# Kernel tuning notes

Hardware: AMD Instinct MI355X
Metric: run time of the kernel (lower is better)

## Reference

```python
import jax, jax.numpy as jnp
import numpy as np

N_NODES = 100000
N_EDGES = 3200000
IN_DIM = 512
HEADS = 4
C1 = 8   # conv1 per-head channels
C2 = 4   # conv2 per-head channels
OUT_DIM = 10
N_GRAPHS = 64
NEG_SLOPE = 0.2


def _leaky_relu(x):
    return jnp.where(x >= 0, x, NEG_SLOPE * x)


def gat_conv(x, src, dst, W, a_src, a_dst, b):
    """PyG GATConv (concat=True). x:[N,F], src/dst:[E], W:[F,H*C], a_*:[H,C], b:[H*C]."""
    N = x.shape[0]
    H, C = a_src.shape
    h = (x @ W).reshape(N, H, C)                      # [N,H,C]
    e_src = jnp.einsum('nhc,hc->nh', h, a_src)        # [N,H]
    e_dst = jnp.einsum('nhc,hc->nh', h, a_dst)
    e = _leaky_relu(e_src[src] + e_dst[dst])          # [E,H]
    # segment softmax over edges grouped by destination node
    m = jax.ops.segment_max(e, dst, num_segments=N)   # [N,H]
    ex = jnp.exp(e - m[dst])
    denom = jax.ops.segment_sum(ex, dst, num_segments=N)
    alpha = ex / (denom[dst] + 1e-16)                 # [E,H]
    out = jax.ops.segment_sum(h[src] * alpha[:, :, None], dst, num_segments=N)
    return out.reshape(N, H * C) + b


def setup_inputs() -> dict:
    key = jax.random.key(0)
    ks = jax.random.split(key, 16)
    x = jax.random.normal(ks[0], (N_NODES, IN_DIM), dtype=jnp.float32)
    edge_index = jax.random.randint(ks[1], (2, N_EDGES), 0, N_NODES, dtype=jnp.int64)
    batch = jnp.sort(jax.random.randint(ks[2], (N_NODES,), 0, N_GRAPHS, dtype=jnp.int64))
    def glorot(k, shape):
        fan_in = shape[0] if len(shape) == 2 else shape[-1]
        return jax.random.normal(k, shape, dtype=jnp.float32) * (1.0 / np.sqrt(fan_in))
    return {
        'x': x, 'edge_index': edge_index, 'batch': batch,
        'W1': glorot(ks[3], (IN_DIM, HEADS * C1)),
        'att_src1': glorot(ks[4], (HEADS, C1)),
        'att_dst1': glorot(ks[5], (HEADS, C1)),
        'b1': jnp.zeros((HEADS * C1,), jnp.float32),
        'W2': glorot(ks[6], (HEADS * C1, HEADS * C2)),
        'att_src2': glorot(ks[7], (HEADS, C2)),
        'att_dst2': glorot(ks[8], (HEADS, C2)),
        'b2': jnp.zeros((HEADS * C2,), jnp.float32),
        'Wf': glorot(ks[9], (HEADS * C2, OUT_DIM)),
        'bf': jnp.zeros((OUT_DIM,), jnp.float32),
    }


def reference(x, edge_index, batch, W1, att_src1, att_dst1, b1,
              W2, att_src2, att_dst2, b2, Wf, bf):
    N = x.shape[0]
    loops = jnp.arange(N, dtype=edge_index.dtype)     # add_self_loops=True
    src = jnp.concatenate([edge_index[0], loops])
    dst = jnp.concatenate([edge_index[1], loops])
    h = jax.nn.relu(gat_conv(x, src, dst, W1, att_src1, att_dst1, b1))
    h = jax.nn.relu(gat_conv(h, src, dst, W2, att_src2, att_dst2, b2))
    # global_mean_pool over graphs
    sums = jax.ops.segment_sum(h, batch, num_segments=N_GRAPHS)
    cnt = jax.ops.segment_sum(jnp.ones((N,), h.dtype), batch, num_segments=N_GRAPHS)
    pooled = sums / jnp.maximum(cnt, 1.0)[:, None]    # [G, 16]
    return pooled @ Wf + bf
```

## Files before the change

### kernel.cpp

```cpp
#include <hip/hip_runtime.h>


#define LRELU(v) ((v) >= 0.f ? (v) : 0.2f * (v))

__global__ __launch_bounds__(256) void k_bin(const int* __restrict__ ei,
                                             int2* __restrict__ stg,
                                             int* __restrict__ rcnt,
                                             int E0, int Etot, int nr, int cap) {
    __shared__ int cnt[1024];
    __shared__ int base[1024];
    const int t = threadIdx.x;
    for (int i = t; i < nr; i += 256) cnt[i] = 0;
    __syncthreads();
    const int e0 = blockIdx.x * 8192;
#pragma unroll 4
    for (int k = 0; k < 32; k++) {
        int e = e0 + k * 256 + t;
        if (e < Etot) {
            int d = (e < E0) ? ei[E0 + e] : (e - E0);
            atomicAdd(&cnt[d >> 8], 1);
        }
    }
    __syncthreads();
    for (int i = t; i < nr; i += 256) {
        int c = cnt[i];
        base[i] = c ? atomicAdd(&rcnt[i], c) : 0;
        cnt[i] = 0;
    }
    __syncthreads();
#pragma unroll 4
    for (int k = 0; k < 32; k++) {
        int e = e0 + k * 256 + t;
        if (e < Etot) {
            int s, d;
            if (e < E0) {
                s = ei[e];
                d = ei[E0 + e];
            } else {
                s = d = e - E0;
            }
            int r = d >> 8;
            int slot = base[r] + atomicAdd(&cnt[r], 1);
            stg[(size_t)r * cap + slot] = make_int2(s, d);
        }
    }
}

__global__ __launch_bounds__(512) void k_sort(const int2* __restrict__ stg,
                                              const int* __restrict__ rcnt,
                                              int* __restrict__ row_ptr,
                                              int* __restrict__ ssrc,
                                              int N, int Etot, int nr, int cap) {
    __shared__ int hist[256];
    __shared__ int hs[256];
    __shared__ int red[512];
    const int r = blockIdx.x;
    const int t = threadIdx.x;
    int part = 0;
    for (int i = t; i < r; i += 512) part += rcnt[i];
    red[t] = part;
    if (t < 256) hist[t] = 0;
    __syncthreads();
    for (int off = 256; off > 0; off >>= 1) {
        if (t < off) red[t] += red[t + off];
        __syncthreads();
    }
    const int rb = red[0];
    const int n0 = r << 8;
    const int cnt = rcnt[r];
    const int2* seg = stg + (size_t)r * cap;
    for (int i = t; i < cnt; i += 512) {
        int d = seg[i].y;
        atomicAdd(&hist[d - n0], 1);
    }
    __syncthreads();
    if (t < 256) hs[t] = hist[t];
    __syncthreads();
    for (int off = 1; off < 256; off <<= 1) {
        int o = (t < 256 && t >= off) ? hs[t - off] : 0;
        __syncthreads();
        if (t < 256) hs[t] += o;
        __syncthreads();
    }
    if (t < 256) {
        int excl = hs[t] - hist[t];
        int node = n0 + t;
        if (node < N) row_ptr[node] = rb + excl;
        hist[t] = excl;
    }
    if (r == nr - 1 && t == 0) row_ptr[N] = Etot;
    __syncthreads();
    for (int i = t; i < cnt; i += 512) {
        int2 sd2 = seg[i];
        int off = atomicAdd(&hist[sd2.y - n0], 1);
        ssrc[rb + off] = sd2.x;
    }
}

__global__ __launch_bounds__(256) void k_gemm1(const float* __restrict__ x,
                                               const float* __restrict__ W,
                                               const float* __restrict__ a_src,
                                               const float* __restrict__ a_dst,
                                               float* __restrict__ h,
                                               float* __restrict__ es,
                                               float* __restrict__ ed, int N) {
    __shared__ float xs[32 * 132];
    __shared__ float ws[32 * 36];
    const int t = threadIdx.x;
    const int r0 = (t >> 2) * 2;
    const int cg = t & 3;
    const int row0 = blockIdx.x * 128;

    float acc[2][8];
#pragma unroll
    for (int i = 0; i < 2; i++)
#pragma unroll
        for (int j = 0; j < 8; j++) acc[i][j] = 0.f;

    float4 xr[4];
    float4 wr;
    const int xrow = t >> 3, xc4 = t & 7;
    const int wk = t >> 3, wc4 = t & 7;

    auto load_chunk = [&](int kc) {
#pragma unroll
        for (int ii = 0; ii < 4; ii++) {
            int row = xrow + ii * 32;
            int rr = row0 + row;
            if (rr >= N) rr = N - 1;
            xr[ii] = *(const float4*)&x[(size_t)rr * 512 + kc + xc4 * 4];
        }
        wr = *(const float4*)&W[(size_t)(kc + wk) * 32 + wc4 * 4];
    };

    load_chunk(0);
    for (int c = 0; c < 16; c++) {
        __syncthreads();
#pragma unroll
        for (int ii = 0; ii < 4; ii++) {
            int row = xrow + ii * 32;
            xs[(xc4 * 4 + 0) * 132 + row] = xr[ii].x;
            xs[(xc4 * 4 + 1) * 132 + row] = xr[ii].y;
            xs[(xc4 * 4 + 2) * 132 + row] = xr[ii].z;
            xs[(xc4 * 4 + 3) * 132 + row] = xr[ii].w;
        }
        ws[wk * 36 + wc4 * 4 + 0] = wr.x;
        ws[wk * 36 + wc4 * 4 + 1] = wr.y;
        ws[wk * 36 + wc4 * 4 + 2] = wr.z;
        ws[wk * 36 + wc4 * 4 + 3] = wr.w;
        __syncthreads();
        if (c < 15) load_chunk((c + 1) * 32);
#pragma unroll 8
        for (int k = 0; k < 32; k++) {
            float2 xv = *(const float2*)&xs[k * 132 + r0];
            float4 w0 = *(const float4*)&ws[k * 36 + cg * 8];
            float4 w1 = *(const float4*)&ws[k * 36 + cg * 8 + 4];
            acc[0][0] += xv.x * w0.x;
            acc[0][1] += xv.x * w0.y;
            acc[0][2] += xv.x * w0.z;
            acc[0][3] += xv.x * w0.w;
            acc[0][4] += xv.x * w1.x;
            acc[0][5] += xv.x * w1.y;
            acc[0][6] += xv.x * w1.z;
            acc[0][7] += xv.x * w1.w;
            acc[1][0] += xv.y * w0.x;
            acc[1][1] += xv.y * w0.y;
            acc[1][2] += xv.y * w0.z;
            acc[1][3] += xv.y * w0.w;
            acc[1][4] += xv.y * w1.x;
            acc[1][5] += xv.y * w1.y;
            acc[1][6] += xv.y * w1.z;
            acc[1][7] += xv.y * w1.w;
        }
    }

    float4 as0 = *(const float4*)&a_src[cg * 8];
    float4 as1 = *(const float4*)&a_src[cg * 8 + 4];
    float4 ad0 = *(const float4*)&a_dst[cg * 8];
    float4 ad1 = *(const float4*)&a_dst[cg * 8 + 4];
#pragma unroll
    for (int i = 0; i < 2; i++) {
        int r = row0 + r0 + i;
        if (r < N) {
            *(float4*)&h[(size_t)r * 32 + cg * 8] =
                make_float4(acc[i][0], acc[i][1], acc[i][2], acc[i][3]);
            *(float4*)&h[(size_t)r * 32 + cg * 8 + 4] =
                make_float4(acc[i][4], acc[i][5], acc[i][6], acc[i][7]);
            es[r * 4 + cg] = acc[i][0] * as0.x + acc[i][1] * as0.y +
                             acc[i][2] * as0.z + acc[i][3] * as0.w +
                             acc[i][4] * as1.x + acc[i][5] * as1.y +
                             acc[i][6] * as1.z + acc[i][7] * as1.w;
            ed[r * 4 + cg] = acc[i][0] * ad0.x + acc[i][1] * ad0.y +
                             acc[i][2] * ad0.z + acc[i][3] * ad0.w +
                             acc[i][4] * ad1.x + acc[i][5] * ad1.y +
                             acc[i][6] * ad1.z + acc[i][7] * ad1.w;
        }
    }
}

__global__ __launch_bounds__(256) void k_agg1(const int* __restrict__ row_ptr,
                                              const int* __restrict__ ssrc,
                                              const float* __restrict__ hsrc,
                                              const float* __restrict__ es,
                                              const float* __restrict__ ed,
                                              const float* __restrict__ bias,
                                              const float* __restrict__ W2,
                                              const float* __restrict__ a2s,
                                              const float* __restrict__ a2d,
                                              float* __restrict__ h2,
                                              float* __restrict__ es2,
                                              float* __restrict__ ed2, int N) {
    constexpr int U = 8;
    __shared__ float w2s[512];
    __shared__ float b1s[32];
    __shared__ float a2ss[16], a2ds[16];
    const int t = threadIdx.x;
    for (int i = t; i < 512; i += 256) w2s[i] = W2[i];
    if (t < 32) b1s[t] = bias[t];
    if (t < 16) { a2ss[t] = a2s[t]; a2ds[t] = a2d[t]; }
    __syncthreads();

    const int lane = t & 63;
    const int d = blockIdx.x * 4 + (t >> 6);
    if (d >= N) return;
    const int c = lane & 31;
    const int e2 = lane >> 5;
    const int hh = c >> 3;
    const int start = row_ptr[d];
    const int deg = row_ptr[d + 1] - start;
    const float edh = ed[d * 4 + hh];
    const int j0 = (e2 < deg) ? e2 : 0;

    float l = 0.f, acc = 0.f;
    for (int jb = e2; jb < deg; jb += U * 2) {
        int sv[U];
        float wv[U];
#pragma unroll
        for (int u = 0; u < U; u++) {
            int jj = jb + u * 2;
            bool ok = jj < deg;
            wv[u] = ok ? 1.f : 0.f;
            sv[u] = ssrc[start + (ok ? jj : j0)];
        }
        float hv[U];
#pragma unroll
        for (int u = 0; u < U; u++) hv[u] = hsrc[(size_t)sv[u] * 32 + c];
        float pv[U];
#pragma unroll
        for (int u = 0; u < U; u++) {
            float ev = es[sv[u] * 4 + hh] + edh;
            ev = LRELU(ev);
            pv[u] = __expf(ev) * wv[u];
        }
#pragma unroll
        for (int u = 0; u < U; u++) {
            l += pv[u];
            acc += pv[u] * hv[u];
        }
    }
#pragma unroll
    for (int off = 32; off < 64; off <<= 1) {
        l += __shfl_xor(l, off);
        acc += __shfl_xor(acc, off);
    }
    float v = acc / (l + 1e-16f) + b1s[c];
    v = v > 0.f ? v : 0.f;

    const int q = lane & 15;
    float h2q = 0.f;
#pragma unroll
    for (int cc = 0; cc < 32; cc++) {
        float gv = __shfl(v, cc);
        h2q += gv * w2s[cc * 16 + q];
    }
    float p1 = h2q * a2ss[q];
    float p2 = h2q * a2ds[q];
    p1 += __shfl_xor(p1, 1);
    p1 += __shfl_xor(p1, 2);
    p2 += __shfl_xor(p2, 1);
    p2 += __shfl_xor(p2, 2);
    if (lane < 16) {
        h2[(size_t)d * 16 + q] = h2q;
        if ((lane & 3) == 0) {
            es2[d * 4 + (lane >> 2)] = p1;
            ed2[d * 4 + (lane >> 2)] = p2;
        }
    }
}

template <int HC>
__global__ __launch_bounds__(256) void k_agg(const int* __restrict__ row_ptr,
                                             const int* __restrict__ ssrc,
                                             const float* __restrict__ hsrc,
                                             const float* __restrict__ es,
                                             const float* __restrict__ ed,
                                             const float* __restrict__ bias,
                                             float* __restrict__ out, int N) {
    constexpr int E2 = 64 / HC;
    constexpr int U = 8;
    const int lane = threadIdx.x & 63;
    const int d = blockIdx.x * 4 + (threadIdx.x >> 6);
    if (d >= N) return;
    const int c = lane & (HC - 1);
    const int e2 = lane / HC;
    const int hh = c / (HC / 4);
    const int start = row_ptr[d];
    const int deg = row_ptr[d + 1] - start;
    const float edh = ed[d * 4 + hh];
    const int j0 = (e2 < deg) ? e2 : 0;

    float l = 0.f, acc = 0.f;
    for (int jb = e2; jb < deg; jb += U * E2) {
        int sv[U];
        float wv[U];
#pragma unroll
        for (int u = 0; u < U; u++) {
            int jj = jb + u * E2;
            bool ok = jj < deg;
            wv[u] = ok ? 1.f : 0.f;
            sv[u] = ssrc[start + (ok ? jj : j0)];
        }
        float hv[U];
#pragma unroll
        for (int u = 0; u < U; u++) hv[u] = hsrc[(size_t)sv[u] * HC + c];
        float pv[U];
#pragma unroll
        for (int u = 0; u < U; u++) {
            float ev = es[sv[u] * 4 + hh] + edh;
            ev = LRELU(ev);
            pv[u] = __expf(ev) * wv[u];
        }
#pragma unroll
        for (int u = 0; u < U; u++) {
            l += pv[u];
            acc += pv[u] * hv[u];
        }
    }
#pragma unroll
    for (int off = HC; off < 64; off <<= 1) {
        l += __shfl_xor(l, off);
        acc += __shfl_xor(acc, off);
    }
    if (lane < HC) {
        float v = acc / (l + 1e-16f) + bias[c];
        out[(size_t)d * HC + c] = v > 0.f ? v : 0.f;
    }
}

__global__ __launch_bounds__(256) void k_final(const float* __restrict__ h3,
                                               const int* __restrict__ batch,
                                               const float* __restrict__ Wf,
                                               const float* __restrict__ bf,
                                               float* __restrict__ out, int N) {
    __shared__ float part[16][17];
    __shared__ float pooled[16];
    int g = blockIdx.x;
    int t = threadIdx.x;

    int lo = 0, b = N;
    while (lo < b) { int mid = (lo + b) >> 1; if (batch[mid] < g) lo = mid + 1; else b = mid; }
    int hi = lo; b = N;
    while (hi < b) { int mid = (hi + b) >> 1; if (batch[mid] < g + 1) hi = mid + 1; else b = mid; }

    int ch = t & 15, r = t >> 4;
    float acc = 0.f;
    for (int i = lo + r; i < hi; i += 16) acc += h3[(size_t)i * 16 + ch];
    part[r][ch] = acc;
    __syncthreads();
    if (t < 16) {
        float s = 0.f;
#pragma unroll
        for (int rr = 0; rr < 16; rr++) s += part[rr][t];
        float cnt = (float)(hi - lo);
        pooled[t] = s / fmaxf(cnt, 1.f);
    }
    __syncthreads();
    if (t < 10) {
        float v = bf[t];
#pragma unroll
        for (int cc = 0; cc < 16; cc++) v += pooled[cc] * Wf[cc * 10 + t];
        out[g * 10 + t] = v;
    }
}

extern "C" void kernel_launch(void* const* d_in, const int* in_sizes, int n_in,
                              void* d_out, int out_size, void* d_ws, size_t ws_size,
                              hipStream_t stream) {
    const float* x   = (const float*)d_in[0];
    const int*   ei  = (const int*)d_in[1];
    const int*   bat = (const int*)d_in[2];
    const float* W1  = (const float*)d_in[3];
    const float* as1 = (const float*)d_in[4];
    const float* ad1 = (const float*)d_in[5];
    const float* b1  = (const float*)d_in[6];
    const float* W2  = (const float*)d_in[7];
    const float* as2 = (const float*)d_in[8];
    const float* ad2 = (const float*)d_in[9];
    const float* b2  = (const float*)d_in[10];
    const float* Wf  = (const float*)d_in[11];
    const float* bf  = (const float*)d_in[12];
    float* outp = (float*)d_out;

    const int N = in_sizes[2];
    const int E0 = in_sizes[1] / 2;
    const int Etot = E0 + N;
    const int nr = (N + 255) >> 8;
    const int cap = Etot / nr + 2048;

    char* w = (char*)d_ws;
    auto alloc = [&](size_t bytes) -> char* {
        char* p = w;
        w += (bytes + 255) & ~(size_t)255;
        return p;
    };
    float* h1  = (float*)alloc((size_t)N * 32 * 4);
    float* es1 = (float*)alloc((size_t)N * 4 * 4);
    float* ed1 = (float*)alloc((size_t)N * 4 * 4);
    float* h2  = (float*)alloc((size_t)N * 16 * 4);
    float* es2 = (float*)alloc((size_t)N * 4 * 4);
    float* ed2 = (float*)alloc((size_t)N * 4 * 4);
    int* rcnt    = (int*)alloc(4096);
    int* row_ptr = (int*)alloc((size_t)(N + 1) * 4);
    int* ssrc    = (int*)alloc((size_t)Etot * 4);
    int2* stg    = (int2*)alloc((size_t)nr * cap * 8);
    float* h3 = h1;

    const int nb1 = (N + 127) / 128;

    hipMemsetAsync(rcnt, 0, 4096, stream);
    k_bin<<<(Etot + 8191) / 8192, 256, 0, stream>>>(ei, stg, rcnt, E0, Etot, nr, cap);
    k_sort<<<nr, 512, 0, stream>>>(stg, rcnt, row_ptr, ssrc, N, Etot, nr, cap);
    k_gemm1<<<nb1, 256, 0, stream>>>(x, W1, as1, ad1, h1, es1, ed1, N);
    k_agg1<<<(N + 3) / 4, 256, 0, stream>>>(row_ptr, ssrc, h1, es1, ed1, b1,
                                            W2, as2, ad2, h2, es2, ed2, N);
    k_agg<16><<<(N + 3) / 4, 256, 0, stream>>>(row_ptr, ssrc, h2, es2, ed2, b2, h3, N);
    k_final<<<64, 256, 0, stream>>>(h3, bat, Wf, bf, outp, N);
}
```

Before: 627.5 us.

## Split node features into head-major planes and aggregate per head

Node features and attention logits now use a head-major layout, [head][node][C] instead of [node][head*C]. Aggregation runs one head per block (C lanes per edge, more edges per wave), so each head's gathered working set is smaller and more cache-friendly. The fused layer-2 projection is split out of the layer-1 aggregation into a separate shared-memory GEMM kernel. This adds a launch and an extra round trip for the intermediate buffer, and the per-head gathers repeat the index loads once per head.

```diff
diff --git a/kernel.cpp b/kernel.cpp
--- a/kernel.cpp
+++ b/kernel.cpp
@@ -182,131 +182,45 @@
     for (int i = 0; i < 2; i++) {
         int r = row0 + r0 + i;
         if (r < N) {
-            *(float4*)&h[(size_t)r * 32 + cg * 8] =
+            float* hrow = h + ((size_t)cg * N + r) * 8;
+            *(float4*)&hrow[0] =
                 make_float4(acc[i][0], acc[i][1], acc[i][2], acc[i][3]);
-            *(float4*)&h[(size_t)r * 32 + cg * 8 + 4] =
+            *(float4*)&hrow[4] =
                 make_float4(acc[i][4], acc[i][5], acc[i][6], acc[i][7]);
-            es[r * 4 + cg] = acc[i][0] * as0.x + acc[i][1] * as0.y +
-                             acc[i][2] * as0.z + acc[i][3] * as0.w +
-                             acc[i][4] * as1.x + acc[i][5] * as1.y +
-                             acc[i][6] * as1.z + acc[i][7] * as1.w;
-            ed[r * 4 + cg] = acc[i][0] * ad0.x + acc[i][1] * ad0.y +
-                             acc[i][2] * ad0.z + acc[i][3] * ad0.w +
-                             acc[i][4] * ad1.x + acc[i][5] * ad1.y +
-                             acc[i][6] * ad1.z + acc[i][7] * ad1.w;
-        }
-    }
-}
-
-__global__ __launch_bounds__(256) void k_agg1(const int* __restrict__ row_ptr,
+            es[(size_t)cg * N + r] = acc[i][0] * as0.x + acc[i][1] * as0.y +
+                                     acc[i][2] * as0.z + acc[i][3] * as0.w +
+                                     acc[i][4] * as1.x + acc[i][5] * as1.y +
+                                     acc[i][6] * as1.z + acc[i][7] * as1.w;
+            ed[(size_t)cg * N + r] = acc[i][0] * ad0.x + acc[i][1] * ad0.y +
+                                     acc[i][2] * ad0.z + acc[i][3] * ad0.w +
+                                     acc[i][4] * ad1.x + acc[i][5] * ad1.y +
+                                     acc[i][6] * ad1.z + acc[i][7] * ad1.w;
+        }
+    }
+}
+
+template <int C, int U>
+__global__ __launch_bounds__(256) void k_aggh(const int* __restrict__ row_ptr,
                                               const int* __restrict__ ssrc,
-                                              const float* __restrict__ hsrc,
-                                              const float* __restrict__ es,
-                                              const float* __restrict__ ed,
+                                              const float* __restrict__ hbase,
+                                              const float* __restrict__ esb,
+                                              const float* __restrict__ edb,
                                               const float* __restrict__ bias,
-                                              const float* __restrict__ W2,
-                                              const float* __restrict__ a2s,
-                                              const float* __restrict__ a2d,
-                                              float* __restrict__ h2,
-                                              float* __restrict__ es2,
-                                              float* __restrict__ ed2, int N) {
-    constexpr int U = 8;
-    __shared__ float w2s[512];
-    __shared__ float b1s[32];
-    __shared__ float a2ss[16], a2ds[16];
-    const int t = threadIdx.x;
-    for (int i = t; i < 512; i += 256) w2s[i] = W2[i];
-    if (t < 32) b1s[t] = bias[t];
-    if (t < 16) { a2ss[t] = a2s[t]; a2ds[t] = a2d[t]; }
-    __syncthreads();
-
-    const int lane = t & 63;
-    const int d = blockIdx.x * 4 + (t >> 6);
+                                              float* __restrict__ outb, int N) {
+    constexpr int E2 = 64 / C;
+    const int b = blockIdx.x;
+    const int head = (b & 7) >> 1;
+    const int g = (b >> 3) * 2 + (b & 1);
+    const int lane = threadIdx.x & 63;
+    const int d = g * 4 + (threadIdx.x >> 6);
     if (d >= N) return;
-    const int c = lane & 31;
-    const int e2 = lane >> 5;
-    const int hh = c >> 3;
+    const float* __restrict__ hh = hbase + (size_t)head * N * C;
+    const float* __restrict__ esh = esb + (size_t)head * N;
+    const int c = lane & (C - 1);
+    const int e2 = lane / C;
     const int start = row_ptr[d];
     const int deg = row_ptr[d + 1] - start;
-    const float edh = ed[d * 4 + hh];
-    const int j0 = (e2 < deg) ? e2 : 0;
-
-    float l = 0.f, acc = 0.f;
-    for (int jb = e2; jb < deg; jb += U * 2) {
-        int sv[U];
-        float wv[U];
-#pragma unroll
-        for (int u = 0; u < U; u++) {
-            int jj = jb + u * 2;
-            bool ok = jj < deg;
-            wv[u] = ok ? 1.f : 0.f;
-            sv[u] = ssrc[start + (ok ? jj : j0)];
-        }
-        float hv[U];
-#pragma unroll
-        for (int u = 0; u < U; u++) hv[u] = hsrc[(size_t)sv[u] * 32 + c];
-        float pv[U];
-#pragma unroll
-        for (int u = 0; u < U; u++) {
-            float ev = es[sv[u] * 4 + hh] + edh;
-            ev = LRELU(ev);
-            pv[u] = __expf(ev) * wv[u];
-        }
-#pragma unroll
-        for (int u = 0; u < U; u++) {
-            l += pv[u];
-            acc += pv[u] * hv[u];
-        }
-    }
-#pragma unroll
-    for (int off = 32; off < 64; off <<= 1) {
-        l += __shfl_xor(l, off);
-        acc += __shfl_xor(acc, off);
-    }
-    float v = acc / (l + 1e-16f) + b1s[c];
-    v = v > 0.f ? v : 0.f;
-
-    const int q = lane & 15;
-    float h2q = 0.f;
-#pragma unroll
-    for (int cc = 0; cc < 32; cc++) {
-        float gv = __shfl(v, cc);
-        h2q += gv * w2s[cc * 16 + q];
-    }
-    float p1 = h2q * a2ss[q];
-    float p2 = h2q * a2ds[q];
-    p1 += __shfl_xor(p1, 1);
-    p1 += __shfl_xor(p1, 2);
-    p2 += __shfl_xor(p2, 1);
-    p2 += __shfl_xor(p2, 2);
-    if (lane < 16) {
-        h2[(size_t)d * 16 + q] = h2q;
-        if ((lane & 3) == 0) {
-            es2[d * 4 + (lane >> 2)] = p1;
-            ed2[d * 4 + (lane >> 2)] = p2;
-        }
-    }
-}
-
-template <int HC>
-__global__ __launch_bounds__(256) void k_agg(const int* __restrict__ row_ptr,
-                                             const int* __restrict__ ssrc,
-                                             const float* __restrict__ hsrc,
-                                             const float* __restrict__ es,
-                                             const float* __restrict__ ed,
-                                             const float* __restrict__ bias,
-                                             float* __restrict__ out, int N) {
-    constexpr int E2 = 64 / HC;
-    constexpr int U = 8;
-    const int lane = threadIdx.x & 63;
-    const int d = blockIdx.x * 4 + (threadIdx.x >> 6);
-    if (d >= N) return;
-    const int c = lane & (HC - 1);
-    const int e2 = lane / HC;
-    const int hh = c / (HC / 4);
-    const int start = row_ptr[d];
-    const int deg = row_ptr[d + 1] - start;
-    const float edh = ed[d * 4 + hh];
+    const float edh = edb[(size_t)head * N + d];
     const int j0 = (e2 < deg) ? e2 : 0;
 
     float l = 0.f, acc = 0.f;
@@ -322,11 +236,11 @@
         }
         float hv[U];
 #pragma unroll
-        for (int u = 0; u < U; u++) hv[u] = hsrc[(size_t)sv[u] * HC + c];
+        for (int u = 0; u < U; u++) hv[u] = hh[(size_t)sv[u] * C + c];
         float pv[U];
 #pragma unroll
         for (int u = 0; u < U; u++) {
-            float ev = es[sv[u] * 4 + hh] + edh;
+            float ev = esh[sv[u]] + edh;
             ev = LRELU(ev);
             pv[u] = __expf(ev) * wv[u];
         }
@@ -337,14 +251,67 @@
         }
     }
 #pragma unroll
-    for (int off = HC; off < 64; off <<= 1) {
+    for (int off = C; off < 64; off <<= 1) {
         l += __shfl_xor(l, off);
         acc += __shfl_xor(acc, off);
     }
-    if (lane < HC) {
-        float v = acc / (l + 1e-16f) + bias[c];
-        out[(size_t)d * HC + c] = v > 0.f ? v : 0.f;
-    }
+    if (lane < C) {
+        float v = acc / (l + 1e-16f) + bias[head * C + c];
+        outb[((size_t)head * N + d) * C + c] = v > 0.f ? v : 0.f;
+    }
+}
+
+__global__ __launch_bounds__(256) void k_gemm2(const float* __restrict__ g1,
+                                               const float* __restrict__ W2,
+                                               const float* __restrict__ a2s,
+                                               const float* __restrict__ a2d,
+                                               float* __restrict__ h2,
+                                               float* __restrict__ es2,
+                                               float* __restrict__ ed2, int N) {
+    __shared__ float rows[64 * 33];
+    __shared__ float w2s[512];
+    const int t = threadIdx.x;
+    const int n0 = blockIdx.x * 64;
+#pragma unroll
+    for (int hh = 0; hh < 4; hh++) {
+        int node = t >> 2, c2 = (t & 3) * 2;
+        int n = n0 + node;
+        if (n >= N) n = N - 1;
+        float2 v = *(const float2*)&g1[((size_t)hh * N + n) * 8 + c2];
+        rows[node * 33 + hh * 8 + c2] = v.x;
+        rows[node * 33 + hh * 8 + c2 + 1] = v.y;
+    }
+    if (t < 128) {
+        float4 v = *(const float4*)&W2[t * 4];
+        w2s[t * 4 + 0] = v.x;
+        w2s[t * 4 + 1] = v.y;
+        w2s[t * 4 + 2] = v.z;
+        w2s[t * 4 + 3] = v.w;
+    }
+    __syncthreads();
+    const int oh = t >> 6, node = t & 63;
+    const int n = n0 + node;
+    if (n >= N) return;
+    float acc[4] = {0.f, 0.f, 0.f, 0.f};
+#pragma unroll 8
+    for (int cc = 0; cc < 32; cc++) {
+        float v = rows[node * 33 + cc];
+        float4 w = *(const float4*)&w2s[cc * 16 + oh * 4];
+        acc[0] += v * w.x;
+        acc[1] += v * w.y;
+        acc[2] += v * w.z;
+        acc[3] += v * w.w;
+    }
+    *(float4*)&h2[((size_t)oh * N + n) * 4] =
+        make_float4(acc[0], acc[1], acc[2], acc[3]);
+    float s1 = 0.f, s2 = 0.f;
+#pragma unroll
+    for (int j = 0; j < 4; j++) {
+        s1 += acc[j] * a2s[oh * 4 + j];
+        s2 += acc[j] * a2d[oh * 4 + j];
+    }
+    es2[(size_t)oh * N + n] = s1;
+    ed2[(size_t)oh * N + n] = s2;
 }
 
 __global__ __launch_bounds__(256) void k_final(const float* __restrict__ h3,
@@ -363,8 +330,9 @@
     while (hi < b) { int mid = (hi + b) >> 1; if (batch[mid] < g + 1) hi = mid + 1; else b = mid; }
 
     int ch = t & 15, r = t >> 4;
+    int hh = ch >> 2, c = ch & 3;
     float acc = 0.f;
-    for (int i = lo + r; i < hi; i += 16) acc += h3[(size_t)i * 16 + ch];
+    for (int i = lo + r; i < hi; i += 16) acc += h3[((size_t)hh * N + i) * 4 + c];
     part[r][ch] = acc;
     __syncthreads();
     if (t < 16) {
@@ -413,26 +381,28 @@
         w += (bytes + 255) & ~(size_t)255;
         return p;
     };
-    float* h1  = (float*)alloc((size_t)N * 32 * 4);
+    float* h1h = (float*)alloc((size_t)N * 32 * 4);
     float* es1 = (float*)alloc((size_t)N * 4 * 4);
     float* ed1 = (float*)alloc((size_t)N * 4 * 4);
-    float* h2  = (float*)alloc((size_t)N * 16 * 4);
+    float* g1h = (float*)alloc((size_t)N * 32 * 4);
+    float* h2h = (float*)alloc((size_t)N * 16 * 4);
     float* es2 = (float*)alloc((size_t)N * 4 * 4);
     float* ed2 = (float*)alloc((size_t)N * 4 * 4);
     int* rcnt    = (int*)alloc(4096);
     int* row_ptr = (int*)alloc((size_t)(N + 1) * 4);
     int* ssrc    = (int*)alloc((size_t)Etot * 4);
     int2* stg    = (int2*)alloc((size_t)nr * cap * 8);
-    float* h3 = h1;
+    float* h3h = h1h;
 
     const int nb1 = (N + 127) / 128;
+    const int cph = (N + 7) / 8;
 
     hipMemsetAsync(rcnt, 0, 4096, stream);
     k_bin<<<(Etot + 8191) / 8192, 256, 0, stream>>>(ei, stg, rcnt, E0, Etot, nr, cap);
     k_sort<<<nr, 512, 0, stream>>>(stg, rcnt, row_ptr, ssrc, N, Etot, nr, cap);
-    k_gemm1<<<nb1, 256, 0, stream>>>(x, W1, as1, ad1, h1, es1, ed1, N);
-    k_agg1<<<(N + 3) / 4, 256, 0, stream>>>(row_ptr, ssrc, h1, es1, ed1, b1,
-                                            W2, as2, ad2, h2, es2, ed2, N);
-    k_agg<16><<<(N + 3) / 4, 256, 0, stream>>>(row_ptr, ssrc, h2, es2, ed2, b2, h3, N);
-    k_final<<<64, 256, 0, stream>>>(h3, bat, Wf, bf, outp, N);
-}
+    k_gemm1<<<nb1, 256, 0, stream>>>(x, W1, as1, ad1, h1h, es1, ed1, N);
+    k_aggh<8, 8><<<8 * cph, 256, 0, stream>>>(row_ptr, ssrc, h1h, es1, ed1, b1, g1h, N);
+    k_gemm2<<<(N + 63) / 64, 256, 0, stream>>>(g1h, W2, as2, ad2, h2h, es2, ed2, N);
+    k_aggh<4, 4><<<8 * cph, 256, 0, stream>>>(row_ptr, ssrc, h2h, es2, ed2, b2, h3h, N);
+    k_final<<<64, 256, 0, stream>>>(h3h, bat, Wf, bf, outp, N);
+}
```

Result: slower. 769.1 us (+22.6%).

## Precompute per-edge attention weights in separate pass and split layer-2 GEMM out

Applied to the files above, without the earlier changes.

Adds a per-edge kernel that computes exp(leaky_relu(es[src]+ed[dst])) for all four heads into a float4 array, using a new sorted destination array written by the sort kernel. The aggregation kernels then read these precomputed weights instead of gathering es per edge and recomputing exp per channel lane. The fused layer-1 aggregate plus W2 projection is split into a generic aggregation and a separate small GEMM kernel. This removes redundant exp and gather work but adds a large per-edge buffer (16 bytes per edge), extra sdst writes, and two extra launches with their global-memory traffic.

```diff
diff --git a/kernel.cpp b/kernel.cpp
--- a/kernel.cpp
+++ b/kernel.cpp
@@ -50,6 +50,7 @@
                                               const int* __restrict__ rcnt,
                                               int* __restrict__ row_ptr,
                                               int* __restrict__ ssrc,
+                                              int* __restrict__ sdst,
                                               int N, int Etot, int nr, int cap) {
     __shared__ int hist[256];
     __shared__ int hs[256];
@@ -94,6 +95,7 @@
         int2 sd2 = seg[i];
         int off = atomicAdd(&hist[sd2.y - n0], 1);
         ssrc[rb + off] = sd2.x;
+        sdst[rb + off] = sd2.y;
     }
 }
 
@@ -198,102 +200,31 @@
     }
 }
 
-__global__ __launch_bounds__(256) void k_agg1(const int* __restrict__ row_ptr,
-                                              const int* __restrict__ ssrc,
-                                              const float* __restrict__ hsrc,
-                                              const float* __restrict__ es,
-                                              const float* __restrict__ ed,
-                                              const float* __restrict__ bias,
-                                              const float* __restrict__ W2,
-                                              const float* __restrict__ a2s,
-                                              const float* __restrict__ a2d,
-                                              float* __restrict__ h2,
-                                              float* __restrict__ es2,
-                                              float* __restrict__ ed2, int N) {
-    constexpr int U = 8;
-    __shared__ float w2s[512];
-    __shared__ float b1s[32];
-    __shared__ float a2ss[16], a2ds[16];
-    const int t = threadIdx.x;
-    for (int i = t; i < 512; i += 256) w2s[i] = W2[i];
-    if (t < 32) b1s[t] = bias[t];
-    if (t < 16) { a2ss[t] = a2s[t]; a2ds[t] = a2d[t]; }
-    __syncthreads();
-
-    const int lane = t & 63;
-    const int d = blockIdx.x * 4 + (t >> 6);
-    if (d >= N) return;
-    const int c = lane & 31;
-    const int e2 = lane >> 5;
-    const int hh = c >> 3;
-    const int start = row_ptr[d];
-    const int deg = row_ptr[d + 1] - start;
-    const float edh = ed[d * 4 + hh];
-    const int j0 = (e2 < deg) ? e2 : 0;
-
-    float l = 0.f, acc = 0.f;
-    for (int jb = e2; jb < deg; jb += U * 2) {
-        int sv[U];
-        float wv[U];
-#pragma unroll
-        for (int u = 0; u < U; u++) {
-            int jj = jb + u * 2;
-            bool ok = jj < deg;
-            wv[u] = ok ? 1.f : 0.f;
-            sv[u] = ssrc[start + (ok ? jj : j0)];
-        }
-        float hv[U];
-#pragma unroll
-        for (int u = 0; u < U; u++) hv[u] = hsrc[(size_t)sv[u] * 32 + c];
-        float pv[U];
-#pragma unroll
-        for (int u = 0; u < U; u++) {
-            float ev = es[sv[u] * 4 + hh] + edh;
-            ev = LRELU(ev);
-            pv[u] = __expf(ev) * wv[u];
-        }
-#pragma unroll
-        for (int u = 0; u < U; u++) {
-            l += pv[u];
-            acc += pv[u] * hv[u];
-        }
-    }
-#pragma unroll
-    for (int off = 32; off < 64; off <<= 1) {
-        l += __shfl_xor(l, off);
-        acc += __shfl_xor(acc, off);
-    }
-    float v = acc / (l + 1e-16f) + b1s[c];
-    v = v > 0.f ? v : 0.f;
-
-    const int q = lane & 15;
-    float h2q = 0.f;
-#pragma unroll
-    for (int cc = 0; cc < 32; cc++) {
-        float gv = __shfl(v, cc);
-        h2q += gv * w2s[cc * 16 + q];
-    }
-    float p1 = h2q * a2ss[q];
-    float p2 = h2q * a2ds[q];
-    p1 += __shfl_xor(p1, 1);
-    p1 += __shfl_xor(p1, 2);
-    p2 += __shfl_xor(p2, 1);
-    p2 += __shfl_xor(p2, 2);
-    if (lane < 16) {
-        h2[(size_t)d * 16 + q] = h2q;
-        if ((lane & 3) == 0) {
-            es2[d * 4 + (lane >> 2)] = p1;
-            ed2[d * 4 + (lane >> 2)] = p2;
-        }
-    }
+__global__ __launch_bounds__(256) void k_alpha(const int* __restrict__ ssrc,
+                                               const int* __restrict__ sdst,
+                                               const float* __restrict__ es,
+                                               const float* __restrict__ ed,
+                                               float4* __restrict__ alf, int Etot) {
+    int i = blockIdx.x * 256 + threadIdx.x;
+    if (i >= Etot) return;
+    int s = ssrc[i];
+    int d = sdst[i];
+    float4 a = *(const float4*)&es[(size_t)s * 4];
+    float4 b = *(const float4*)&ed[(size_t)d * 4];
+    float4 o;
+    float v;
+    v = a.x + b.x; o.x = __expf(LRELU(v));
+    v = a.y + b.y; o.y = __expf(LRELU(v));
+    v = a.z + b.z; o.z = __expf(LRELU(v));
+    v = a.w + b.w; o.w = __expf(LRELU(v));
+    alf[i] = o;
 }
 
 template <int HC>
 __global__ __launch_bounds__(256) void k_agg(const int* __restrict__ row_ptr,
                                              const int* __restrict__ ssrc,
                                              const float* __restrict__ hsrc,
-                                             const float* __restrict__ es,
-                                             const float* __restrict__ ed,
+                                             const float4* __restrict__ alf,
                                              const float* __restrict__ bias,
                                              float* __restrict__ out, int N) {
     constexpr int E2 = 64 / HC;
@@ -306,34 +237,33 @@
     const int hh = c / (HC / 4);
     const int start = row_ptr[d];
     const int deg = row_ptr[d + 1] - start;
-    const float edh = ed[d * 4 + hh];
     const int j0 = (e2 < deg) ? e2 : 0;
 
     float l = 0.f, acc = 0.f;
     for (int jb = e2; jb < deg; jb += U * E2) {
-        int sv[U];
+        int idx[U];
         float wv[U];
 #pragma unroll
         for (int u = 0; u < U; u++) {
             int jj = jb + u * E2;
             bool ok = jj < deg;
             wv[u] = ok ? 1.f : 0.f;
-            sv[u] = ssrc[start + (ok ? jj : j0)];
-        }
+            idx[u] = start + (ok ? jj : j0);
+        }
+        int sv[U];
+#pragma unroll
+        for (int u = 0; u < U; u++) sv[u] = ssrc[idx[u]];
+        float av[U];
+#pragma unroll
+        for (int u = 0; u < U; u++)
+            av[u] = ((const float*)&alf[idx[u]])[hh] * wv[u];
         float hv[U];
 #pragma unroll
         for (int u = 0; u < U; u++) hv[u] = hsrc[(size_t)sv[u] * HC + c];
-        float pv[U];
 #pragma unroll
         for (int u = 0; u < U; u++) {
-            float ev = es[sv[u] * 4 + hh] + edh;
-            ev = LRELU(ev);
-            pv[u] = __expf(ev) * wv[u];
-        }
-#pragma unroll
-        for (int u = 0; u < U; u++) {
-            l += pv[u];
-            acc += pv[u] * hv[u];
+            l += av[u];
+            acc += av[u] * hv[u];
         }
     }
 #pragma unroll
@@ -345,6 +275,61 @@
         float v = acc / (l + 1e-16f) + bias[c];
         out[(size_t)d * HC + c] = v > 0.f ? v : 0.f;
     }
+}
+
+__global__ __launch_bounds__(256) void k_gemm2(const float* __restrict__ g1,
+                                               const float* __restrict__ W2,
+                                               const float* __restrict__ a2s,
+                                               const float* __restrict__ a2d,
+                                               float* __restrict__ h2,
+                                               float* __restrict__ es2,
+                                               float* __restrict__ ed2, int N) {
+    __shared__ float rows[64 * 33];
+    __shared__ float ws[32 * 20];
+    int t = threadIdx.x;
+    int n0 = blockIdx.x * 64;
+#pragma unroll
+    for (int ii = 0; ii < 2; ii++) {
+        int idx = ii * 256 + t;
+        int node = idx >> 3, c4 = idx & 7;
+        float4 v = make_float4(0.f, 0.f, 0.f, 0.f);
+        if (n0 + node < N) v = *(const float4*)&g1[(size_t)(n0 + node) * 32 + c4 * 4];
+        rows[node * 33 + c4 * 4 + 0] = v.x;
+        rows[node * 33 + c4 * 4 + 1] = v.y;
+        rows[node * 33 + c4 * 4 + 2] = v.z;
+        rows[node * 33 + c4 * 4 + 3] = v.w;
+    }
+    if (t < 128) {
+        int r = t >> 2, c4 = t & 3;
+        float4 v = *(const float4*)&W2[r * 16 + c4 * 4];
+        ws[r * 20 + c4 * 4 + 0] = v.x;
+        ws[r * 20 + c4 * 4 + 1] = v.y;
+        ws[r * 20 + c4 * 4 + 2] = v.z;
+        ws[r * 20 + c4 * 4 + 3] = v.w;
+    }
+    __syncthreads();
+    int node = t >> 2, q = t & 3;
+    int n = n0 + node;
+    if (n >= N) return;
+    float acc[4] = {0.f, 0.f, 0.f, 0.f};
+#pragma unroll 8
+    for (int cc = 0; cc < 32; cc++) {
+        float v = rows[node * 33 + cc];
+        float4 w = *(const float4*)&ws[cc * 20 + q * 4];
+        acc[0] += v * w.x;
+        acc[1] += v * w.y;
+        acc[2] += v * w.z;
+        acc[3] += v * w.w;
+    }
+    *(float4*)&h2[(size_t)n * 16 + q * 4] = make_float4(acc[0], acc[1], acc[2], acc[3]);
+    float s1 = 0.f, s2 = 0.f;
+#pragma unroll
+    for (int j = 0; j < 4; j++) {
+        s1 += acc[j] * a2s[q * 4 + j];
+        s2 += acc[j] * a2d[q * 4 + j];
+    }
+    es2[n * 4 + q] = s1;
+    ed2[n * 4 + q] = s2;
 }
 
 __global__ __launch_bounds__(256) void k_final(const float* __restrict__ h3,
@@ -416,23 +401,29 @@
     float* h1  = (float*)alloc((size_t)N * 32 * 4);
     float* es1 = (float*)alloc((size_t)N * 4 * 4);
     float* ed1 = (float*)alloc((size_t)N * 4 * 4);
+    float* g1  = (float*)alloc((size_t)N * 32 * 4);
     float* h2  = (float*)alloc((size_t)N * 16 * 4);
     float* es2 = (float*)alloc((size_t)N * 4 * 4);
     float* ed2 = (float*)alloc((size_t)N * 4 * 4);
     int* rcnt    = (int*)alloc(4096);
     int* row_ptr = (int*)alloc((size_t)(N + 1) * 4);
     int* ssrc    = (int*)alloc((size_t)Etot * 4);
+    int* sdst    = (int*)alloc((size_t)Etot * 4);
+    float4* alf  = (float4*)alloc((size_t)Etot * 16);
     int2* stg    = (int2*)alloc((size_t)nr * cap * 8);
     float* h3 = h1;
 
     const int nb1 = (N + 127) / 128;
+    const int nbe = (Etot + 255) / 256;
 
     hipMemsetAsync(rcnt, 0, 4096, stream);
     k_bin<<<(Etot + 8191) / 8192, 256, 0, stream>>>(ei, stg, rcnt, E0, Etot, nr, cap);
-    k_sort<<<nr, 512, 0, stream>>>(stg, rcnt, row_ptr, ssrc, N, Etot, nr, cap);
+    k_sort<<<nr, 512, 0, stream>>>(stg, rcnt, row_ptr, ssrc, sdst, N, Etot, nr, cap);
     k_gemm1<<<nb1, 256, 0, stream>>>(x, W1, as1, ad1, h1, es1, ed1, N);
-    k_agg1<<<(N + 3) / 4, 256, 0, stream>>>(row_ptr, ssrc, h1, es1, ed1, b1,
-                                            W2, as2, ad2, h2, es2, ed2, N);
-    k_agg<16><<<(N + 3) / 4, 256, 0, stream>>>(row_ptr, ssrc, h2, es2, ed2, b2, h3, N);
+    k_alpha<<<nbe, 256, 0, stream>>>(ssrc, sdst, es1, ed1, alf, Etot);
+    k_agg<32><<<(N + 3) / 4, 256, 0, stream>>>(row_ptr, ssrc, h1, alf, b1, g1, N);
+    k_gemm2<<<(N + 63) / 64, 256, 0, stream>>>(g1, W2, as2, ad2, h2, es2, ed2, N);
+    k_alpha<<<nbe, 256, 0, stream>>>(ssrc, sdst, es2, ed2, alf, Etot);
+    k_agg<16><<<(N + 3) / 4, 256, 0, stream>>>(row_ptr, ssrc, h2, alf, b2, h3, N);
     k_final<<<64, 256, 0, stream>>>(h3, bat, Wf, bf, outp, N);
 }
```

New measurement: 660.4 us. 1.05x slower.
